# Optimization experiments

Measured on AMD Instinct MI355X. Metric: run time of the kernel, lower is better.

Reference implementation:

```python
import jax, jax.numpy as jnp
import numpy as np
import math

B, S, HID = 2, 2048, 1024
NUM_HEADS = 16
HEAD_DIM = HID // NUM_HEADS
SPARSITY_RATIO = 0.1
NEG = -1e9


def _make_sparse_mask(key, seq_len, sparsity_ratio):
    # local window: min(32, seq_len // 4), rows attend to |i - j| <= window // 2
    local_window = min(32, seq_len // 4)
    half = local_window // 2
    idx = jnp.arange(seq_len)
    mask = jnp.abs(idx[:, None] - idx[None, :]) <= half  # [S, S] bool
    # random global connections: n_global random columns per row
    n_global = int(seq_len * sparsity_ratio)
    gidx = jax.random.randint(key, (seq_len, n_global), 0, seq_len)
    mask = mask.at[idx[:, None], gidx].set(True)
    return mask


def setup_inputs() -> dict:
    key = jax.random.key(0)
    ks = jax.random.split(key, 6)
    lim = math.sqrt(6.0 / (HID + HID))  # xavier uniform bound
    def w(k):
        return jax.random.uniform(k, (HID, HID), jnp.float32, -lim, lim)
    return {
        "hidden_states": jax.random.normal(ks[0], (B, S, HID), jnp.float32),
        "Wq": w(ks[1]), "bq": jnp.zeros((HID,), jnp.float32),
        "Wk": w(ks[2]), "bk": jnp.zeros((HID,), jnp.float32),
        "Wv": w(ks[3]), "bv": jnp.zeros((HID,), jnp.float32),
        "Wo": w(ks[4]), "bo": jnp.zeros((HID,), jnp.float32),
        "sparse_mask": _make_sparse_mask(ks[5], S, SPARSITY_RATIO),
    }


def reference(hidden_states, Wq, bq, Wk, bk, Wv, bv, Wo, bo, sparse_mask):
    Bsz, seq, hid = hidden_states.shape
    H, D = NUM_HEADS, hid // NUM_HEADS

    def proj(W, b):
        y = hidden_states @ W.T + b                      # [B, S, hid]
        return y.reshape(Bsz, seq, H, D).transpose(0, 2, 1, 3)  # [B, H, S, D]

    q = proj(Wq, bq)
    k = proj(Wk, bk)
    v = proj(Wv, bv)

    scores = jnp.einsum("bhqd,bhkd->bhqk", q, k) / jnp.sqrt(jnp.float32(D))
    scores = jnp.where(sparse_mask[None, None, :, :], scores, jnp.float32(NEG))
    probs = jax.nn.softmax(scores, axis=-1)
    ctx = jnp.einsum("bhqk,bhkd->bhqd", probs, v)        # [B, H, S, D]
    ctx = ctx.transpose(0, 2, 1, 3).reshape(Bsz, seq, hid)
    return ctx @ Wo.T + bo
```

## Files before the change

### kernel.cpp

```cpp
#include <hip/hip_runtime.h>

typedef short bf16x8 __attribute__((ext_vector_type(8)));
typedef float f32x4 __attribute__((ext_vector_type(4)));
typedef unsigned short us4 __attribute__((ext_vector_type(4)));

#define S_LEN 2048
#define HIDD 1024
#define NH 16
#define HD 64

#define BK 64

static __device__ __forceinline__ unsigned short f2bf(float f) {
  union { float f; unsigned u; } v; v.f = f;
  unsigned r = v.u + 0x7FFFu + ((v.u >> 16) & 1u);
  return (unsigned short)(r >> 16);
}

static __device__ __forceinline__ float bf2f(unsigned short u) {
  union { unsigned u; float f; } v; v.u = ((unsigned)u) << 16;
  return v.f;
}

static __device__ __forceinline__ unsigned cvtpk(float lo, float hi) {
  unsigned r;
  asm("v_cvt_pk_bf16_f32 %0, %1, %2" : "=v"(r) : "v"(lo), "v"(hi));
  return r;
}

static __device__ __forceinline__ float ex2(float x) {
#if __has_builtin(__builtin_amdgcn_exp2f)
  return __builtin_amdgcn_exp2f(x);
#else
  return __expf(x * 0.69314718056f);
#endif
}

#define GLD16(gp, lp)                                                        \
  __builtin_amdgcn_global_load_lds(                                         \
      (const __attribute__((address_space(1))) void*)(gp),                  \
      (__attribute__((address_space(3))) void*)(lp), 16, 0, 0)

__global__ __launch_bounds__(256) void cvt5_kernel(
    const float* __restrict__ s0, const float* __restrict__ s1, const float* __restrict__ s2,
    const float* __restrict__ s3, const float* __restrict__ s4,
    unsigned short* __restrict__ d0, unsigned short* __restrict__ d1,
    unsigned short* __restrict__ d2, unsigned short* __restrict__ d3,
    unsigned short* __restrict__ d4) {
  const float* s; unsigned short* d; int n4;
  switch (blockIdx.y) {
    case 0: s = s0; d = d0; n4 = (2 * S_LEN * HIDD) / 4; break;
    case 1: s = s1; d = d1; n4 = (HIDD * HIDD) / 4; break;
    case 2: s = s2; d = d2; n4 = (HIDD * HIDD) / 4; break;
    case 3: s = s3; d = d3; n4 = (HIDD * HIDD) / 4; break;
    default: s = s4; d = d4; n4 = (HIDD * HIDD) / 4; break;
  }
  for (int i = blockIdx.x * blockDim.x + threadIdx.x; i < n4;
       i += gridDim.x * blockDim.x) {
    float4 v = ((const float4*)s)[i];
    us4 o;
    o.x = f2bf(v.x); o.y = f2bf(v.y); o.z = f2bf(v.z); o.w = f2bf(v.w);
    ((us4*)d)[i] = o;
  }
}

__global__ __launch_bounds__(256) void maskbits_kernel(
    const unsigned char* __restrict__ m8, unsigned* __restrict__ bits) {
  int idx = blockIdx.x * 256 + threadIdx.x;
  int q = idx >> 6, w = idx & 63;
  bool bytemode = (m8[1] != 0);
  unsigned r = 0;
  if (bytemode) {
    const uint4* p = (const uint4*)(m8 + (size_t)q * 2048 + w * 32);
    uint4 a = p[0], b = p[1];
    unsigned v[8] = {a.x, a.y, a.z, a.w, b.x, b.y, b.z, b.w};
#pragma unroll
    for (int j = 0; j < 8; ++j)
#pragma unroll
      for (int k = 0; k < 4; ++k)
        r |= (((v[j] >> (k * 8)) & 255u) ? 1u : 0u) << (j * 4 + k);
  } else {
    const int4* p = (const int4*)((const int*)m8 + (size_t)q * 2048 + (size_t)w * 32);
#pragma unroll
    for (int j = 0; j < 8; ++j) {
      int4 v = p[j];
      r |= (v.x ? 1u : 0u) << (j * 4 + 0);
      r |= (v.y ? 1u : 0u) << (j * 4 + 1);
      r |= (v.z ? 1u : 0u) << (j * 4 + 2);
      r |= (v.w ? 1u : 0u) << (j * 4 + 3);
    }
  }
  bits[idx] = r;
}

template <int MFRAG>
static __device__ __forceinline__ void gemm_core2(
    const unsigned short* __restrict__ A, const unsigned short* __restrict__ W,
    int bm0, int bn0, unsigned short* As, unsigned short* Bs,
    f32x4 (&acc)[MFRAG][4]) {
  const int tid = threadIdx.x;
  const int lane = tid & 63;
  const int wid = tid >> 6;
  const int wr = wid >> 1, wc = wid & 1;
  const int l15 = lane & 15, g = lane >> 4, l7 = l15 & 7;
  const int ra = (g ^ l7) * 8;

  for (int k0 = 0; k0 < HIDD; k0 += BK) {
    __syncthreads();
#pragma unroll
    for (int it = 0; it < MFRAG; ++it) {
      int p = it * 256 + tid;
      int r = p >> 3, ch = (p & 7) ^ (r & 7);
      GLD16(A + (size_t)(bm0 + r) * HIDD + k0 + ch * 8,
            As + (it * 256 + wid * 64) * 8);
    }
#pragma unroll
    for (int it = 0; it < 4; ++it) {
      int p = it * 256 + tid;
      int r = p >> 3, ch = (p & 7) ^ (r & 7);
      GLD16(W + (size_t)(bn0 + r) * HIDD + k0 + ch * 8,
            Bs + (it * 256 + wid * 64) * 8);
    }
    __syncthreads();
#pragma unroll
    for (int kk = 0; kk < 2; ++kk) {
      bf16x8 af[MFRAG], bfr[4];
#pragma unroll
      for (int m = 0; m < MFRAG; ++m)
        af[m] = *(const bf16x8*)&As[(wr * (MFRAG * 16) + m * 16 + l15) * 64 + (ra ^ (kk * 32))];
#pragma unroll
      for (int n = 0; n < 4; ++n)
        bfr[n] = *(const bf16x8*)&Bs[(wc * 64 + n * 16 + l15) * 64 + (ra ^ (kk * 32))];
#pragma unroll
      for (int m = 0; m < MFRAG; ++m)
#pragma unroll
        for (int n = 0; n < 4; ++n)
          acc[m][n] = __builtin_amdgcn_mfma_f32_16x16x32_bf16(af[m], bfr[n], acc[m][n], 0, 0, 0);
    }
  }
}

__global__ __launch_bounds__(256) void gemm_qkv(
    const unsigned short* __restrict__ hs,
    const unsigned short* __restrict__ Wq, const unsigned short* __restrict__ Wk,
    const unsigned short* __restrict__ Wv,
    const float* __restrict__ bq, const float* __restrict__ bk, const float* __restrict__ bv,
    unsigned short* __restrict__ Qs, unsigned short* __restrict__ Kb,
    unsigned short* __restrict__ VT) {
  __shared__ __align__(16) unsigned short As[128 * 64];
  __shared__ __align__(16) unsigned short Bs[128 * 64];
  const int z = blockIdx.z;
  const unsigned short* W = (z == 0) ? Wq : ((z == 1) ? Wk : Wv);
  const float* bias = (z == 0) ? bq : ((z == 1) ? bk : bv);

  f32x4 acc[4][4];
#pragma unroll
  for (int m = 0; m < 4; ++m)
#pragma unroll
    for (int n = 0; n < 4; ++n) acc[m][n] = (f32x4){0.f, 0.f, 0.f, 0.f};

  const int bm0 = blockIdx.x * 128, bn0 = blockIdx.y * 128;
  gemm_core2<4>(hs, W, bm0, bn0, As, Bs, acc);

  const int lane = threadIdx.x & 63;
  const int wid = threadIdx.x >> 6;
  const int wr = wid >> 1, wc = wid & 1;
  const int l15 = lane & 15, g = lane >> 4;
  const float qscale = 0.125f * 1.44269504088896f;

#pragma unroll
  for (int m = 0; m < 4; ++m) {
#pragma unroll
    for (int n = 0; n < 4; ++n) {
      int grow0 = bm0 + wr * 64 + m * 16 + g * 4;
      int gcol = bn0 + wc * 64 + n * 16 + l15;
      float bv_ = bias[gcol];
      if (z == 0) {
#pragma unroll
        for (int i = 0; i < 4; ++i)
          Qs[(size_t)(grow0 + i) * HIDD + gcol] = f2bf((acc[m][n][i] + bv_) * qscale);
      } else if (z == 1) {
#pragma unroll
        for (int i = 0; i < 4; ++i)
          Kb[(size_t)(grow0 + i) * HIDD + gcol] = f2bf(acc[m][n][i] + bv_);
      } else {
        int b = grow0 >> 11, s = grow0 & 2047;
        int h = gcol >> 6, d = gcol & 63;
        us4 pk;
#pragma unroll
        for (int i = 0; i < 4; ++i) pk[i] = f2bf(acc[m][n][i] + bv_);
        *(us4*)&VT[((size_t)(b * NH + h) * HD + d) * S_LEN + s] = pk;
      }
    }
  }
}

__global__ __launch_bounds__(256) void gemm_o(
    const unsigned short* __restrict__ ctx, const unsigned short* __restrict__ Wo,
    const float* __restrict__ bo, float* __restrict__ out) {
  __shared__ __align__(16) unsigned short As[64 * 64];
  __shared__ __align__(16) unsigned short Bs[128 * 64];
  f32x4 acc[2][4];
#pragma unroll
  for (int m = 0; m < 2; ++m)
#pragma unroll
    for (int n = 0; n < 4; ++n) acc[m][n] = (f32x4){0.f, 0.f, 0.f, 0.f};

  const int bm0 = blockIdx.x * 64, bn0 = blockIdx.y * 128;
  gemm_core2<2>(ctx, Wo, bm0, bn0, As, Bs, acc);

  const int lane = threadIdx.x & 63;
  const int wid = threadIdx.x >> 6;
  const int wr = wid >> 1, wc = wid & 1;
  const int l15 = lane & 15, g = lane >> 4;
#pragma unroll
  for (int m = 0; m < 2; ++m) {
#pragma unroll
    for (int n = 0; n < 4; ++n) {
      int grow0 = bm0 + wr * 32 + m * 16 + g * 4;
      int gcol = bn0 + wc * 64 + n * 16 + l15;
      float bv_ = bo[gcol];
#pragma unroll
      for (int i = 0; i < 4; ++i)
        out[(size_t)(grow0 + i) * HIDD + gcol] = acc[m][n][i] + bv_;
    }
  }
}

__global__ __launch_bounds__(512) void attn5_kernel(
    const unsigned short* __restrict__ Qs, const unsigned short* __restrict__ Kb,
    const unsigned short* __restrict__ VT, const unsigned* __restrict__ mbits,
    unsigned short* __restrict__ part0, unsigned short* __restrict__ part1,
    float2* __restrict__ ml) {
  __shared__ __align__(16) unsigned short Kt[2][4096];
  __shared__ __align__(16) unsigned short Vt[2][4096];
  __shared__ __align__(16) unsigned short Pl[8][16][72];

  const int tid = threadIdx.x;
  const int wid = tid >> 6, lane = tid & 63;
  const int l15 = lane & 15, g = lane >> 4;
  const int l7 = l15 & 7;
  const int b = blockIdx.x >> 4, h = blockIdx.x & 15;
  const int z = blockIdx.z;
  const int kvbase = z * 1024;
  const int qrow = blockIdx.y * 128 + wid * 16 + l15;

  const unsigned short* Kbh = Kb + (size_t)b * S_LEN * HIDD + h * HD;
  const unsigned short* VTbh = VT + (size_t)(b * NH + h) * HD * S_LEN;

  const unsigned short* Qrow = Qs + (size_t)(b * S_LEN + qrow) * HIDD + h * HD;
  bf16x8 qf0 = *(const bf16x8*)(Qrow + g * 8);
  bf16x8 qf1 = *(const bf16x8*)(Qrow + 32 + g * 8);

  const unsigned* mrow = mbits + (size_t)qrow * 64 + z * 32;

  const int rb0 = l15 * 64 + ((g ^ l7)) * 8;
  const int rb1 = l15 * 64 + ((g ^ l7) ^ 4) * 8;

  const bool isK = (wid < 4);
  const int wk = wid & 3;
  int p0 = wk * 128 + lane;
  int p1 = p0 + 64;
  int r0 = p0 >> 3, c0 = (p0 & 7) ^ (r0 & 7);
  int r1 = p1 >> 3, c1 = (p1 & 7) ^ (r1 & 7);
  const unsigned short* gp0;
  const unsigned short* gp1;
  int gstep;
  unsigned short* lp0;
  if (isK) {
    gp0 = Kbh + (size_t)(kvbase + r0) * HIDD + c0 * 8;
    gp1 = Kbh + (size_t)(kvbase + r1) * HIDD + c1 * 8;
    gstep = 64 * HIDD;
    lp0 = &Kt[0][0] + wk * 1024;
  } else {
    gp0 = VTbh + (size_t)r0 * S_LEN + kvbase + c0 * 8;
    gp1 = VTbh + (size_t)r1 * S_LEN + kvbase + c1 * 8;
    gstep = 64;
    lp0 = &Vt[0][0] + wk * 1024;
  }
  unsigned short* lp1 = lp0 + 512;

  float m_run = -1e8f, l_run = 0.f;
  f32x4 oacc[4];
#pragma unroll
  for (int dc = 0; dc < 4; ++dc) oacc[dc] = (f32x4){0.f, 0.f, 0.f, 0.f};

  GLD16(gp0, lp0);
  GLD16(gp1, lp1);
  gp0 += gstep; gp1 += gstep;
  uint2 mw = *(const uint2*)mrow;
  __syncthreads();

  for (int it = 0; it < 16; ++it) {
    const int tb = ((it + 1) & 1) * 4096;
    GLD16(gp0, lp0 + tb);
    GLD16(gp1, lp1 + tb);
    gp0 += gstep; gp1 += gstep;
    uint2 mw_n = *(const uint2*)(mrow + (it + 1) * 2);

    const unsigned short* Kbuf = &Kt[it & 1][0];
    f32x4 sacc[4];
#pragma unroll
    for (int t = 0; t < 4; ++t) {
      sacc[t] = (f32x4){0.f, 0.f, 0.f, 0.f};
      bf16x8 ka = *(const bf16x8*)(Kbuf + t * 1024 + rb0);
      bf16x8 kb2 = *(const bf16x8*)(Kbuf + t * 1024 + rb1);
      sacc[t] = __builtin_amdgcn_mfma_f32_16x16x32_bf16(ka, qf0, sacc[t], 0, 0, 0);
      sacc[t] = __builtin_amdgcn_mfma_f32_16x16x32_bf16(kb2, qf1, sacc[t], 0, 0, 0);
    }

    float t0 = fmaxf(fmaxf(sacc[0][0], sacc[0][1]), sacc[0][2]);
    float t1 = fmaxf(fmaxf(sacc[0][3], sacc[1][0]), sacc[1][1]);
    float t2 = fmaxf(fmaxf(sacc[1][2], sacc[1][3]), sacc[2][0]);
    float t3 = fmaxf(fmaxf(sacc[2][1], sacc[2][2]), sacc[2][3]);
    float t4 = fmaxf(fmaxf(sacc[3][0], sacc[3][1]), sacc[3][2]);
    float t5 = fmaxf(fmaxf(t0, t1), sacc[3][3]);
    float pmax = fmaxf(fmaxf(fmaxf(t2, t3), t4), t5);
    pmax = fmaxf(pmax, __shfl_xor(pmax, 16));
    pmax = fmaxf(pmax, __shfl_xor(pmax, 32));

    if (__any(pmax > m_run + 8.0f)) {
      float m_new = fmaxf(m_run, pmax);
      float corr = ex2(m_run - m_new);
      l_run *= corr;
#pragma unroll
      for (int dc = 0; dc < 4; ++dc) oacc[dc] *= corr;
      m_run = m_new;
    }

    float lsum = 0.f;
#pragma unroll
    for (int t = 0; t < 4; ++t) {
      unsigned word = (t & 2) ? mw.y : mw.x;
      unsigned nib = word >> ((t & 1) * 16 + g * 4);
      float e0 = ex2(sacc[t][0] - m_run);
      float e1 = ex2(sacc[t][1] - m_run);
      float e2 = ex2(sacc[t][2] - m_run);
      float e3 = ex2(sacc[t][3] - m_run);
      float q0 = (nib & 1u) ? e0 : 0.f;
      float q1 = (nib & 2u) ? e1 : 0.f;
      float q2 = (nib & 4u) ? e2 : 0.f;
      float q3 = (nib & 8u) ? e3 : 0.f;
      lsum += (q0 + q1) + (q2 + q3);
      uint2 w2;
      w2.x = cvtpk(q0, q1);
      w2.y = cvtpk(q2, q3);
      *(uint2*)&Pl[wid][l15][t * 16 + g * 4] = w2;
    }
    lsum += __shfl_xor(lsum, 16);
    lsum += __shfl_xor(lsum, 32);
    l_run += lsum;

    bf16x8 pf0 = *(const bf16x8*)&Pl[wid][l15][g * 8];
    bf16x8 pf1 = *(const bf16x8*)&Pl[wid][l15][32 + g * 8];

    const unsigned short* Vbuf = &Vt[it & 1][0];
#pragma unroll
    for (int dc = 0; dc < 4; ++dc) {
      bf16x8 va = *(const bf16x8*)(Vbuf + dc * 1024 + rb0);
      bf16x8 vb = *(const bf16x8*)(Vbuf + dc * 1024 + rb1);
      oacc[dc] = __builtin_amdgcn_mfma_f32_16x16x32_bf16(va, pf0, oacc[dc], 0, 0, 0);
      oacc[dc] = __builtin_amdgcn_mfma_f32_16x16x32_bf16(vb, pf1, oacc[dc], 0, 0, 0);
    }

    mw = mw_n;
    __syncthreads();
  }

  float linv = 1.f / fmaxf(l_run, 1e-37f);
  unsigned short* obase = (z == 0) ? part0 : part1;
  unsigned short* crow = obase + (size_t)(b * S_LEN + qrow) * HIDD + h * HD;
#pragma unroll
  for (int dc = 0; dc < 4; ++dc) {
    uint2 o;
    o.x = cvtpk(oacc[dc][0] * linv, oacc[dc][1] * linv);
    o.y = cvtpk(oacc[dc][2] * linv, oacc[dc][3] * linv);
    *(uint2*)&crow[dc * 16 + g * 4] = o;
  }
  if (g == 0) {
    ml[(size_t)z * (32 * S_LEN) + (size_t)blockIdx.x * S_LEN + qrow] =
        make_float2(m_run, l_run);
  }
}

__global__ __launch_bounds__(256) void combine_kernel(
    const unsigned short* p1, const float2* __restrict__ ml,
    unsigned short* p0 ) {
  int gid = blockIdx.x * 256 + threadIdx.x;
  int r = gid >> 2;
  int dq = (gid & 3) * 16;
  float2 a = ml[r];
  float2 c = ml[65536 + r];
  float m = fmaxf(a.x, c.x);
  float w0 = a.y * ex2(a.x - m);
  float w1 = c.y * ex2(c.x - m);
  float inv = 1.f / (w0 + w1);
  w0 *= inv; w1 *= inv;
  int bh = r >> 11, q = r & 2047;
  int b = bh >> 4, h = bh & 15;
  size_t off = ((size_t)(b * S_LEN + q)) * HIDD + h * HD + dq;
#pragma unroll
  for (int half = 0; half < 2; ++half) {
    bf16x8 o0 = *(const bf16x8*)(p0 + off + half * 8);
    bf16x8 o1 = *(const bf16x8*)(p1 + off + half * 8);
    unsigned res[4];
#pragma unroll
    for (int j = 0; j < 4; ++j) {
      float v0 = w0 * bf2f((unsigned short)o0[2 * j]) + w1 * bf2f((unsigned short)o1[2 * j]);
      float v1 = w0 * bf2f((unsigned short)o0[2 * j + 1]) + w1 * bf2f((unsigned short)o1[2 * j + 1]);
      res[j] = cvtpk(v0, v1);
    }
    uint4 st = {res[0], res[1], res[2], res[3]};
    *(uint4*)(p0 + off + half * 8) = st;
  }
}

extern "C" void kernel_launch(void* const* d_in, const int* in_sizes, int n_in,
                              void* d_out, int out_size, void* d_ws, size_t ws_size,
                              hipStream_t stream) {
  const float* hs = (const float*)d_in[0];
  const float* Wq = (const float*)d_in[1];
  const float* bq = (const float*)d_in[2];
  const float* Wk = (const float*)d_in[3];
  const float* bk = (const float*)d_in[4];
  const float* Wv = (const float*)d_in[5];
  const float* bv = (const float*)d_in[6];
  const float* Wo = (const float*)d_in[7];
  const float* bo = (const float*)d_in[8];
  const unsigned char* mask = (const unsigned char*)d_in[9];

  char* ws = (char*)d_ws;
  unsigned short* hs_bf = (unsigned short*)(ws);
  unsigned short* Wq_bf = (unsigned short*)(ws + (8u << 20));
  unsigned short* Wk_bf = (unsigned short*)(ws + (10u << 20));
  unsigned short* Wv_bf = (unsigned short*)(ws + (12u << 20));
  unsigned short* Wo_bf = (unsigned short*)(ws + (14u << 20));
  unsigned short* Qs    = (unsigned short*)(ws + (16u << 20));
  unsigned short* Kbf   = (unsigned short*)(ws + (24u << 20));
  unsigned short* VT    = (unsigned short*)(ws + (32u << 20));
  unsigned short* ctxb  = (unsigned short*)(ws + (40u << 20));
  unsigned* mbits       = (unsigned*)(ws);
  unsigned short* part1 = (unsigned short*)(ws + (1u << 19));
  float2* ml            = (float2*)(ws + (9u << 20));
  float* out = (float*)d_out;

  cvt5_kernel<<<dim3(256, 5), 256, 0, stream>>>(hs, Wq, Wk, Wv, Wo,
                                                hs_bf, Wq_bf, Wk_bf, Wv_bf, Wo_bf);
  gemm_qkv<<<dim3(32, 8, 3), 256, 0, stream>>>(hs_bf, Wq_bf, Wk_bf, Wv_bf,
                                               bq, bk, bv, Qs, Kbf, VT);
  maskbits_kernel<<<512, 256, 0, stream>>>(mask, mbits);
  attn5_kernel<<<dim3(32, 16, 2), 512, 0, stream>>>(Qs, Kbf, VT, mbits,
                                                    ctxb, part1, ml);
  combine_kernel<<<1024, 256, 0, stream>>>(part1, ml, ctxb);
  gemm_o<<<dim3(64, 8), 256, 0, stream>>>(ctxb, Wo_bf, bo, out);
}
```

Baseline: 146.9 us.

## Keep attention probabilities in registers and use 16x16x16 MFMA for PV

Drops the per-wave LDS staging buffer for the softmax probabilities. The packed bf16 probabilities now feed 16x16x16 bf16 MFMAs directly, since their accumulator layout matches the B operand, and V is read with matching swizzled 4-element loads. The loop is unrolled by two with compile-time buffer indices, and launch bounds ask for higher occupancy. This removes an LDS round trip and frees shared memory, at the cost of twice as many, smaller MFMA instructions and possible register pressure from the occupancy hint.

Result: slower. 203.0 us (+38.2%).

```diff
diff --git a/kernel.cpp b/kernel.cpp
--- a/kernel.cpp
+++ b/kernel.cpp
@@ -1,6 +1,7 @@
 #include <hip/hip_runtime.h>
 
 typedef short bf16x8 __attribute__((ext_vector_type(8)));
+typedef short bf16x4 __attribute__((ext_vector_type(4)));
 typedef float f32x4 __attribute__((ext_vector_type(4)));
 typedef unsigned short us4 __attribute__((ext_vector_type(4)));
 
@@ -33,6 +34,15 @@
   return __builtin_amdgcn_exp2f(x);
 #else
   return __expf(x * 0.69314718056f);
+#endif
+}
+
+static __device__ __forceinline__ f32x4 mfma16(bf16x4 a, bf16x4 b, f32x4 c) {
+#if __has_builtin(__builtin_amdgcn_mfma_f32_16x16x16bf16_1k)
+  return __builtin_amdgcn_mfma_f32_16x16x16bf16_1k(a, b, c, 0, 0, 0);
+#else
+  asm("v_mfma_f32_16x16x16_bf16 %0, %1, %2, %0" : "+v"(c) : "v"(a), "v"(b));
+  return c;
 #endif
 }
 
@@ -227,14 +237,13 @@
   }
 }
 
-__global__ __launch_bounds__(512) void attn5_kernel(
+__global__ __launch_bounds__(512, 8) void attn6_kernel(
     const unsigned short* __restrict__ Qs, const unsigned short* __restrict__ Kb,
     const unsigned short* __restrict__ VT, const unsigned* __restrict__ mbits,
     unsigned short* __restrict__ part0, unsigned short* __restrict__ part1,
     float2* __restrict__ ml) {
   __shared__ __align__(16) unsigned short Kt[2][4096];
   __shared__ __align__(16) unsigned short Vt[2][4096];
-  __shared__ __align__(16) unsigned short Pl[8][16][72];
 
   const int tid = threadIdx.x;
   const int wid = tid >> 6, lane = tid & 63;
@@ -254,8 +263,14 @@
 
   const unsigned* mrow = mbits + (size_t)qrow * 64 + z * 32;
 
-  const int rb0 = l15 * 64 + ((g ^ l7)) * 8;
+  const int rb0 = l15 * 64 + (g ^ l7) * 8;
   const int rb1 = l15 * 64 + ((g ^ l7) ^ 4) * 8;
+
+  const int gh = g >> 1, gl = g & 1;
+  int vta[4];
+#pragma unroll
+  for (int t = 0; t < 4; ++t)
+    vta[t] = l15 * 64 + (((2 * t + gh) ^ l7) * 8) + gl * 4;
 
   const bool isK = (wid < 4);
   const int wk = wid & 3;
@@ -289,83 +304,84 @@
   GLD16(gp1, lp1);
   gp0 += gstep; gp1 += gstep;
   uint2 mw = *(const uint2*)mrow;
+  int kt = 0;
   __syncthreads();
 
-  for (int it = 0; it < 16; ++it) {
-    const int tb = ((it + 1) & 1) * 4096;
-    GLD16(gp0, lp0 + tb);
-    GLD16(gp1, lp1 + tb);
-    gp0 += gstep; gp1 += gstep;
-    uint2 mw_n = *(const uint2*)(mrow + (it + 1) * 2);
-
-    const unsigned short* Kbuf = &Kt[it & 1][0];
-    f32x4 sacc[4];
-#pragma unroll
-    for (int t = 0; t < 4; ++t) {
-      sacc[t] = (f32x4){0.f, 0.f, 0.f, 0.f};
-      bf16x8 ka = *(const bf16x8*)(Kbuf + t * 1024 + rb0);
-      bf16x8 kb2 = *(const bf16x8*)(Kbuf + t * 1024 + rb1);
-      sacc[t] = __builtin_amdgcn_mfma_f32_16x16x32_bf16(ka, qf0, sacc[t], 0, 0, 0);
-      sacc[t] = __builtin_amdgcn_mfma_f32_16x16x32_bf16(kb2, qf1, sacc[t], 0, 0, 0);
-    }
-
-    float t0 = fmaxf(fmaxf(sacc[0][0], sacc[0][1]), sacc[0][2]);
-    float t1 = fmaxf(fmaxf(sacc[0][3], sacc[1][0]), sacc[1][1]);
-    float t2 = fmaxf(fmaxf(sacc[1][2], sacc[1][3]), sacc[2][0]);
-    float t3 = fmaxf(fmaxf(sacc[2][1], sacc[2][2]), sacc[2][3]);
-    float t4 = fmaxf(fmaxf(sacc[3][0], sacc[3][1]), sacc[3][2]);
-    float t5 = fmaxf(fmaxf(t0, t1), sacc[3][3]);
-    float pmax = fmaxf(fmaxf(fmaxf(t2, t3), t4), t5);
-    pmax = fmaxf(pmax, __shfl_xor(pmax, 16));
-    pmax = fmaxf(pmax, __shfl_xor(pmax, 32));
-
-    if (__any(pmax > m_run + 8.0f)) {
-      float m_new = fmaxf(m_run, pmax);
-      float corr = ex2(m_run - m_new);
-      l_run *= corr;
-#pragma unroll
-      for (int dc = 0; dc < 4; ++dc) oacc[dc] *= corr;
-      m_run = m_new;
-    }
-
-    float lsum = 0.f;
-#pragma unroll
-    for (int t = 0; t < 4; ++t) {
-      unsigned word = (t & 2) ? mw.y : mw.x;
-      unsigned nib = word >> ((t & 1) * 16 + g * 4);
-      float e0 = ex2(sacc[t][0] - m_run);
-      float e1 = ex2(sacc[t][1] - m_run);
-      float e2 = ex2(sacc[t][2] - m_run);
-      float e3 = ex2(sacc[t][3] - m_run);
-      float q0 = (nib & 1u) ? e0 : 0.f;
-      float q1 = (nib & 2u) ? e1 : 0.f;
-      float q2 = (nib & 4u) ? e2 : 0.f;
-      float q3 = (nib & 8u) ? e3 : 0.f;
-      lsum += (q0 + q1) + (q2 + q3);
-      uint2 w2;
-      w2.x = cvtpk(q0, q1);
-      w2.y = cvtpk(q2, q3);
-      *(uint2*)&Pl[wid][l15][t * 16 + g * 4] = w2;
-    }
-    lsum += __shfl_xor(lsum, 16);
-    lsum += __shfl_xor(lsum, 32);
-    l_run += lsum;
-
-    bf16x8 pf0 = *(const bf16x8*)&Pl[wid][l15][g * 8];
-    bf16x8 pf1 = *(const bf16x8*)&Pl[wid][l15][32 + g * 8];
-
-    const unsigned short* Vbuf = &Vt[it & 1][0];
-#pragma unroll
-    for (int dc = 0; dc < 4; ++dc) {
-      bf16x8 va = *(const bf16x8*)(Vbuf + dc * 1024 + rb0);
-      bf16x8 vb = *(const bf16x8*)(Vbuf + dc * 1024 + rb1);
-      oacc[dc] = __builtin_amdgcn_mfma_f32_16x16x32_bf16(va, pf0, oacc[dc], 0, 0, 0);
-      oacc[dc] = __builtin_amdgcn_mfma_f32_16x16x32_bf16(vb, pf1, oacc[dc], 0, 0, 0);
-    }
-
-    mw = mw_n;
-    __syncthreads();
-  }
+#define ABODY(BUF)                                                            \
+  {                                                                           \
+    GLD16(gp0, lp0 + ((BUF) ^ 1) * 4096);                                     \
+    GLD16(gp1, lp1 + ((BUF) ^ 1) * 4096);                                     \
+    gp0 += gstep; gp1 += gstep;                                               \
+    uint2 mw_n = *(const uint2*)(mrow + (kt + 1) * 2);   \
+    f32x4 sacc[4];                                                            \
+    _Pragma("unroll")                                                         \
+    for (int t = 0; t < 4; ++t) {                                             \
+      sacc[t] = (f32x4){0.f, 0.f, 0.f, 0.f};                                  \
+      bf16x8 ka = *(const bf16x8*)&Kt[BUF][t * 1024 + rb0];                   \
+      bf16x8 kb2 = *(const bf16x8*)&Kt[BUF][t * 1024 + rb1];                  \
+      sacc[t] = __builtin_amdgcn_mfma_f32_16x16x32_bf16(ka, qf0, sacc[t], 0, 0, 0); \
+      sacc[t] = __builtin_amdgcn_mfma_f32_16x16x32_bf16(kb2, qf1, sacc[t], 0, 0, 0); \
+    }                                                                         \
+    float t0 = fmaxf(fmaxf(sacc[0][0], sacc[0][1]), sacc[0][2]);              \
+    float t1 = fmaxf(fmaxf(sacc[0][3], sacc[1][0]), sacc[1][1]);              \
+    float t2 = fmaxf(fmaxf(sacc[1][2], sacc[1][3]), sacc[2][0]);              \
+    float t3 = fmaxf(fmaxf(sacc[2][1], sacc[2][2]), sacc[2][3]);              \
+    float t4 = fmaxf(fmaxf(sacc[3][0], sacc[3][1]), sacc[3][2]);              \
+    float t5 = fmaxf(fmaxf(t0, t1), sacc[3][3]);                              \
+    float pmax = fmaxf(fmaxf(fmaxf(t2, t3), t4), t5);                         \
+    pmax = fmaxf(pmax, __shfl_xor(pmax, 16));                                 \
+    pmax = fmaxf(pmax, __shfl_xor(pmax, 32));                                 \
+    if (__any(pmax > m_run + 8.0f)) {                                         \
+      float m_new = fmaxf(m_run, pmax);                                       \
+      float corr = ex2(m_run - m_new);                                        \
+      l_run *= corr;                                                          \
+      _Pragma("unroll")                                                       \
+      for (int dc = 0; dc < 4; ++dc) oacc[dc] *= corr;                        \
+      m_run = m_new;                                                          \
+    }                                                                         \
+    float lsum = 0.f;                                                         \
+    bf16x4 pb[4];                                                             \
+    _Pragma("unroll")                                                         \
+    for (int t = 0; t < 4; ++t) {                                             \
+      unsigned word = (t & 2) ? mw.y : mw.x;                                  \
+      unsigned nib = word >> ((t & 1) * 16 + g * 4);                          \
+      float e0 = ex2(sacc[t][0] - m_run);                                     \
+      float e1 = ex2(sacc[t][1] - m_run);                                     \
+      float e2 = ex2(sacc[t][2] - m_run);                                     \
+      float e3 = ex2(sacc[t][3] - m_run);                                     \
+      float q0 = (nib & 1u) ? e0 : 0.f;                                       \
+      float q1 = (nib & 2u) ? e1 : 0.f;                                       \
+      float q2 = (nib & 4u) ? e2 : 0.f;                                       \
+      float q3 = (nib & 8u) ? e3 : 0.f;                                       \
+      lsum += (q0 + q1) + (q2 + q3);                                          \
+      union { unsigned u[2]; bf16x4 v; } pu;                                  \
+      pu.u[0] = cvtpk(q0, q1);                                                \
+      pu.u[1] = cvtpk(q2, q3);                                                \
+      pb[t] = pu.v;                                                           \
+    }                                                                         \
+    lsum += __shfl_xor(lsum, 16);                                             \
+    lsum += __shfl_xor(lsum, 32);                                             \
+    l_run += lsum;                                                            \
+    _Pragma("unroll")                                                         \
+    for (int dc = 0; dc < 4; ++dc) {                                          \
+      f32x4 o = oacc[dc];                                                     \
+      _Pragma("unroll")                                                       \
+      for (int t = 0; t < 4; ++t) {                                           \
+        bf16x4 va = *(const bf16x4*)&Vt[BUF][vta[t] + dc * 1024];             \
+        o = mfma16(va, pb[t], o);                                             \
+      }                                                                       \
+      oacc[dc] = o;                                                           \
+    }                                                                         \
+    mw = mw_n;                                                                \
+    ++kt;                                                                     \
+    __syncthreads();                                                          \
+  }
+
+  for (int h8 = 0; h8 < 8; ++h8) {
+    ABODY(0);
+    ABODY(1);
+  }
+#undef ABODY
 
   float linv = 1.f / fmaxf(l_run, 1e-37f);
   unsigned short* obase = (z == 0) ? part0 : part1;
@@ -449,7 +465,7 @@
   gemm_qkv<<<dim3(32, 8, 3), 256, 0, stream>>>(hs_bf, Wq_bf, Wk_bf, Wv_bf,
                                                bq, bk, bv, Qs, Kbf, VT);
   maskbits_kernel<<<512, 256, 0, stream>>>(mask, mbits);
-  attn5_kernel<<<dim3(32, 16, 2), 512, 0, stream>>>(Qs, Kbf, VT, mbits,
+  attn6_kernel<<<dim3(32, 16, 2), 512, 0, stream>>>(Qs, Kbf, VT, mbits,
                                                     ctxb, part1, ml);
   combine_kernel<<<1024, 256, 0, stream>>>(part1, ml, ctxb);
   gemm_o<<<dim3(64, 8), 256, 0, stream>>>(ctxb, Wo_bf, bo, out);
```
